# Optimization experiments

Hardware: AMD Instinct MI355X
Metric: run time of the kernel (lower is better)

The kernel has to match this reference:

```python
import jax, jax.numpy as jnp
import numpy as np

B, S, HID = 2, 2048, 1024
H, D = 16, 64
NUM_BUCKETS, MAX_DIST = 32, 128
NEG_INF = -1e9


def _rel_buckets(rel_pos, num_buckets, max_distance):
    # decoder (unidirectional): only non-positive relative positions valid
    rp = -jnp.minimum(rel_pos, 0)  # [q,k] >= 0
    max_exact = num_buckets // 2
    is_small = rp < max_exact
    safe = jnp.maximum(rp, 1).astype(jnp.float32)
    large = max_exact + (
        jnp.log(safe / max_exact) / np.log(max_distance / max_exact) * (num_buckets - max_exact)
    ).astype(jnp.int32)
    large = jnp.minimum(large, num_buckets - 1)
    return jnp.where(is_small, rp, large)


def _rotate_half(t):
    t1, t2 = jnp.split(t, 2, axis=-1)
    return jnp.concatenate([-t2, t1], axis=-1)


def setup_inputs() -> dict:
    key = jax.random.key(0)
    ks = jax.random.split(key, 6)
    sc = 0.02
    x = jax.random.normal(ks[0], (B, S, HID), jnp.float32)
    Wq = jax.random.normal(ks[1], (HID, H * D), jnp.float32) * sc
    Wk = jax.random.normal(ks[2], (HID, H * D), jnp.float32) * sc
    Wv = jax.random.normal(ks[3], (HID, H * D), jnp.float32) * sc
    Wo = jax.random.normal(ks[4], (H * D, HID), jnp.float32) * sc
    rel_bias = jax.random.normal(ks[5], (NUM_BUCKETS, H), jnp.float32) * sc
    # rotary tables: emb = cat(freqs, freqs), non-interleave layout
    inv_freq = 1.0 / (10000.0 ** (np.arange(0, D, 2, dtype=np.float32) / D))
    freqs = np.arange(S, dtype=np.float32)[:, None] * inv_freq[None, :]  # [S, D/2]
    emb = np.concatenate([freqs, freqs], axis=-1)  # [S, D]
    cos = jnp.asarray(np.cos(emb), jnp.float32)
    sin = jnp.asarray(np.sin(emb), jnp.float32)
    return {"x": x, "Wq": Wq, "Wk": Wk, "Wv": Wv, "Wo": Wo,
            "rel_bias": rel_bias, "cos": cos, "sin": sin}


def reference(x, Wq, Wk, Wv, Wo, rel_bias, cos, sin):
    # QKV projections (weights stored [in, out])
    q = (x @ Wq).reshape(B, S, H, D)
    k = (x @ Wk).reshape(B, S, H, D)
    v = (x @ Wv).reshape(B, S, H, D)
    # RoPE (non-interleave): q*cos + rotate_half(q)*sin, cos/sin broadcast over B,H
    c = cos[None, :, None, :]
    s = sin[None, :, None, :]
    q = q * c + _rotate_half(q) * s
    k = k * c + _rotate_half(k) * s
    # scores [B,H,S,S]
    scores = jnp.einsum("bqhd,bkhd->bhqk", q, k) / np.sqrt(D).astype(np.float32)
    # learned relative-position bucket bias (T5-style, decoder/unidirectional)
    ctx_pos = jnp.arange(S)[:, None]
    mem_pos = jnp.arange(S)[None, :]
    buckets = _rel_buckets(mem_pos - ctx_pos, NUM_BUCKETS, MAX_DIST)  # [S,S]
    bias = rel_bias[buckets]  # [S,S,H]
    scores = scores + jnp.transpose(bias, (2, 0, 1))[None]
    # causal mask (decoder self-attention)
    causal = mem_pos <= ctx_pos  # [S,S]
    scores = jnp.where(causal[None, None], scores, NEG_INF)
    attn = jax.nn.softmax(scores, axis=-1)
    ctx = jnp.einsum("bhqk,bkhd->bqhd", attn, v).reshape(B, S, H * D)
    return ctx @ Wo
```

## Files before the change

kernel.cpp:

```cpp
#include <hip/hip_runtime.h>
#include <hip/hip_bf16.h>
#include <math.h>

#define B_   2
#define S_   2048
#define HID_ 1024
#define H_   16
#define D_   64

typedef __attribute__((ext_vector_type(8))) short bf16x8;
typedef __attribute__((ext_vector_type(4))) short bf16x4;
typedef __attribute__((ext_vector_type(4))) float f32x4;
typedef __attribute__((ext_vector_type(4))) unsigned uint4v;
typedef unsigned short u16;

#define LOG2E 1.44269504088896f

static __device__ __forceinline__ u16 f2bf(float f) {
    unsigned u = __builtin_bit_cast(unsigned, f);
    u += 0x7fffu + ((u >> 16) & 1u);
    return (u16)(u >> 16);
}
static __device__ __forceinline__ unsigned cvtpk(float lo, float hi) {
    unsigned r;
    asm("v_cvt_pk_bf16_f32 %0, %1, %2" : "=v"(r) : "v"(lo), "v"(hi));
    return r;
}
static __device__ __forceinline__ int swzK(int row, int colbytes) {
    return row * 128 + (colbytes ^ ((row & 7) << 4));
}
static __device__ __forceinline__ int swzV(int row, int colbytes) {
    return row * 128 + (colbytes ^ ((row & 7) << 4) ^ (((row >> 3) & 1) << 3));
}
static __device__ __forceinline__ void gll16(const void* g, void* l) {
    __builtin_amdgcn_global_load_lds(
        (const __attribute__((address_space(1))) unsigned int*)g,
        (__attribute__((address_space(3))) unsigned int*)l, 16, 0, 0);
}

__global__ __launch_bounds__(256) void convert_x(const float* __restrict__ in,
                                                 u16* __restrict__ out) {
    int i = blockIdx.x * 256 + threadIdx.x;
    float4 f = ((const float4*)in)[i];
    ushort4 u;
    u.x = f2bf(f.x); u.y = f2bf(f.y); u.z = f2bf(f.z); u.w = f2bf(f.w);
    ((ushort4*)out)[i] = u;
}

__global__ __launch_bounds__(256) void transpose_w4(const float* __restrict__ W0,
                                                    const float* __restrict__ W1,
                                                    const float* __restrict__ W2,
                                                    const float* __restrict__ W3,
                                                    u16* __restrict__ o0,
                                                    u16* __restrict__ o1,
                                                    u16* __restrict__ o2,
                                                    u16* __restrict__ o3) {
    __shared__ float tS[32][33];
    const int z = blockIdx.z;
    const float* in = z == 0 ? W0 : z == 1 ? W1 : z == 2 ? W2 : W3;
    u16* out       = z == 0 ? o0 : z == 1 ? o1 : z == 2 ? o2 : o3;
    const int x = threadIdx.x, y = threadIdx.y;
    const int bx = blockIdx.x * 32, by = blockIdx.y * 32;
    #pragma unroll
    for (int j = 0; j < 4; j++)
        tS[y + j * 8][x] = in[(long)(by + y + j * 8) * HID_ + bx + x];
    __syncthreads();
    #pragma unroll
    for (int j = 0; j < 4; j++)
        out[(long)(bx + y + j * 8) * HID_ + by + x] = f2bf(tS[x][y + j * 8]);
}

__global__ __launch_bounds__(256, 3) void gemm_qkv(const u16* __restrict__ A,
                                                   const u16* __restrict__ Bt,
                                                   u16* __restrict__ outb,
                                                   const float* __restrict__ cosb,
                                                   const float* __restrict__ sinb,
                                                   int K) {
    __shared__ u16 As[128 * 32];
    __shared__ u16 Bs[128 * 32];
    const int t = threadIdx.x;
    const int lane = t & 63;
    const int w = t >> 6;
    const int qlane = lane & 15, grp = lane >> 4;
    const int m0 = blockIdx.y * 128, n0 = blockIdx.x * 128;
    const int wr = w >> 1, wc = w & 1;

    f32x4 acc[4][4];
    #pragma unroll
    for (int i = 0; i < 4; i++)
        #pragma unroll
        for (int j = 0; j < 4; j++) acc[i][j] = (f32x4){0.f, 0.f, 0.f, 0.f};

    const int srow = (lane >> 2);
    const int scol = (lane & 3) * 8;
    const int nkt = K >> 5;
    for (int kt = 0; kt < nkt; kt++) {
        const int k0 = kt << 5;
        #pragma unroll
        for (int c = 0; c < 2; c++) {
            const int chunk = w * 2 + c;
            const int row = chunk * 16 + srow;
            gll16(A  + (long)(m0 + row) * K + k0 + scol, As + chunk * 512);
            gll16(Bt + (long)(n0 + row) * K + k0 + scol, Bs + chunk * 512);
        }
        __syncthreads();
        bf16x8 af[4], bfr[4];
        #pragma unroll
        for (int i = 0; i < 4; i++) {
            af[i]  = *(const bf16x8*)(As + (wr * 64 + i * 16 + qlane) * 32 + grp * 8);
            bfr[i] = *(const bf16x8*)(Bs + (wc * 64 + i * 16 + qlane) * 32 + grp * 8);
        }
        #pragma unroll
        for (int mf = 0; mf < 4; mf++)
            #pragma unroll
            for (int nf = 0; nf < 4; nf++)
                acc[mf][nf] = __builtin_amdgcn_mfma_f32_16x16x32_bf16(af[mf], bfr[nf], acc[mf][nf], 0, 0, 0);
        __syncthreads();
    }

    const int gnb = n0 + wc * 64;
    #pragma unroll
    for (int mf = 0; mf < 4; mf++) {
        #pragma unroll
        for (int r = 0; r < 4; r++) {
            const int m = m0 + wr * 64 + mf * 16 + grp * 4 + r;
            float a0 = acc[mf][0][r], a1 = acc[mf][1][r];
            float a2 = acc[mf][2][r], a3 = acc[mf][3][r];
            if (gnb < 2048) {
                const int s = m & (S_ - 1);
                const float* cr = cosb + s * 64;
                const float* sr = sinb + s * 64;
                float c0 = cr[qlane], c1 = cr[qlane + 16], c2 = cr[qlane + 32], c3 = cr[qlane + 48];
                float z0 = sr[qlane], z1 = sr[qlane + 16], z2 = sr[qlane + 32], z3 = sr[qlane + 48];
                float n0v = a0 * c0 - a2 * z0;
                float n1v = a1 * c1 - a3 * z1;
                float n2v = a2 * c2 + a0 * z2;
                float n3v = a3 * c3 + a1 * z3;
                if (gnb < 1024) {
                    const float QS = 0.125f * LOG2E;
                    n0v *= QS; n1v *= QS; n2v *= QS; n3v *= QS;
                }
                a0 = n0v; a1 = n1v; a2 = n2v; a3 = n3v;
            }
            const float av[4] = {a0, a1, a2, a3};
            #pragma unroll
            for (int nf = 0; nf < 4; nf++) {
                const int gn = gnb + nf * 16 + qlane;
                outb[((long)(gn >> 10)) * ((long)4096 * 1024) + (long)m * 1024 + (gn & 1023)]
                    = f2bf(av[nf]);
            }
        }
    }
}

__global__ __launch_bounds__(256, 3) void gemm_n64(const u16* __restrict__ A,
                                                   const u16* __restrict__ Bt,
                                                   float* __restrict__ outf,
                                                   int K) {
    __shared__ u16 As[128 * 32];
    __shared__ u16 Bs[64 * 32];
    const int t = threadIdx.x;
    const int lane = t & 63;
    const int w = t >> 6;
    const int qlane = lane & 15, grp = lane >> 4;
    const int m0 = blockIdx.y * 128, n0 = blockIdx.x * 64;

    f32x4 acc[2][4];
    #pragma unroll
    for (int i = 0; i < 2; i++)
        #pragma unroll
        for (int j = 0; j < 4; j++) acc[i][j] = (f32x4){0.f, 0.f, 0.f, 0.f};

    const int srow = (lane >> 2);
    const int scol = (lane & 3) * 8;
    const int nkt = K >> 5;
    for (int kt = 0; kt < nkt; kt++) {
        const int k0 = kt << 5;
        #pragma unroll
        for (int c = 0; c < 2; c++) {
            const int chunk = w * 2 + c;
            const int row = chunk * 16 + srow;
            gll16(A + (long)(m0 + row) * K + k0 + scol, As + chunk * 512);
        }
        gll16(Bt + (long)(n0 + w * 16 + srow) * K + k0 + scol, Bs + w * 512);
        __syncthreads();
        bf16x8 af[2], bfr[4];
        #pragma unroll
        for (int i = 0; i < 2; i++)
            af[i] = *(const bf16x8*)(As + (w * 32 + i * 16 + qlane) * 32 + grp * 8);
        #pragma unroll
        for (int i = 0; i < 4; i++)
            bfr[i] = *(const bf16x8*)(Bs + (i * 16 + qlane) * 32 + grp * 8);
        #pragma unroll
        for (int mf = 0; mf < 2; mf++)
            #pragma unroll
            for (int nf = 0; nf < 4; nf++)
                acc[mf][nf] = __builtin_amdgcn_mfma_f32_16x16x32_bf16(af[mf], bfr[nf], acc[mf][nf], 0, 0, 0);
        __syncthreads();
    }

    #pragma unroll
    for (int mf = 0; mf < 2; mf++)
        #pragma unroll
        for (int r = 0; r < 4; r++) {
            const int m = m0 + w * 32 + mf * 16 + grp * 4 + r;
            #pragma unroll
            for (int nf = 0; nf < 4; nf++)
                outf[(long)m * 1024 + n0 + nf * 16 + qlane] = acc[mf][nf][r];
        }
}

__global__ __launch_bounds__(512, 4) void attn_mfma(const u16* __restrict__ q,
                                                    const u16* __restrict__ k,
                                                    const u16* __restrict__ v,
                                                    const float* __restrict__ rel_bias,
                                                    u16* __restrict__ ctx) {
    __shared__ __align__(16) unsigned char kS[2][8192];
    __shared__ __align__(16) unsigned char vS[2][8192];
    __shared__ float bb[2][192];

    const int t    = threadIdx.x;
    const int lane = t & 63;
    const int w    = t >> 6;
    const int n    = blockIdx.x;
    const int xcd  = n & 7;
    const int hbhi = (n >> 7) & 3;
    int qtb        = (n >> 3) & 15;
    if (hbhi & 2) qtb = 15 - qtb;
    const int hb   = xcd + (hbhi << 3);
    const int h    = hb & 15, b = hb >> 4;
    const int q0   = qtb * 128;
    const int wq   = w * 16;
    const int qlane = lane & 15;
    const int grp   = lane >> 4;

    const long bhbase = ((long)b * S_ * H_ + h) * D_;
    const float bfar  = rel_bias[31 * H_ + h] * LOG2E;

    const int kr  = t >> 3,        kc  = (t & 7) * 8;
    const int vrb = (t >> 5) * 4,  vcp = (t & 31) * 2;

    bf16x8 qf0, qf1;
    {
        const u16* qrow = q + bhbase + (long)(q0 + wq + qlane) * (H_ * D_);
        qf0 = *(const bf16x8*)(qrow + grp * 8);
        qf1 = *(const bf16x8*)(qrow + 32 + grp * 8);
    }

    f32x4 oacc[4];
    #pragma unroll
    for (int db = 0; db < 4; db++) oacc[db] = (f32x4){0.f, 0.f, 0.f, 0.f};
    float m_run = -1.0e30f, l_run = 0.f;

    bf16x8 kreg;
    unsigned vreg[4];
    float breg = 0.f;

    auto prefetch = [&](int k0, bool needb) {
        kreg = *(const bf16x8*)(k + bhbase + (long)(k0 + kr) * (H_ * D_) + kc);
        const u16* vp = v + bhbase + (long)(k0 + vrb) * (H_ * D_) + vcp;
        #pragma unroll
        for (int i = 0; i < 4; i++)
            vreg[i] = *(const unsigned*)(vp + (long)i * (H_ * D_));
        if (needb && t < 192) {
            int rp = (q0 - 63) + t - k0;
            float bv = 0.f;
            if (rp >= 0) {
                int bucket;
                if (rp < 16) bucket = rp;
                else {
                    int lg = (int)(logf((float)rp * 0.0625f) * 7.69437361f);
                    bucket = 16 + lg;
                    if (bucket > 31) bucket = 31;
                }
                bv = rel_bias[bucket * H_ + h] * LOG2E;
            }
            breg = bv;
        }
    };
    auto writetile = [&](int buf, bool needb) {
        *(bf16x8*)(kS[buf] + swzK(kr, kc * 2)) = kreg;
        ushort2 a0 = __builtin_bit_cast(ushort2, vreg[0]);
        ushort2 a1 = __builtin_bit_cast(ushort2, vreg[1]);
        ushort2 a2 = __builtin_bit_cast(ushort2, vreg[2]);
        ushort2 a3 = __builtin_bit_cast(ushort2, vreg[3]);
        ushort4 d0; d0.x = a0.x; d0.y = a1.x; d0.z = a2.x; d0.w = a3.x;
        ushort4 d1; d1.x = a0.y; d1.y = a1.y; d1.z = a2.y; d1.w = a3.y;
        *(ushort4*)(vS[buf] + swzV(vcp,     vrb * 2)) = d0;
        *(ushort4*)(vS[buf] + swzV(vcp + 1, vrb * 2)) = d1;
        if (needb && t < 192) bb[buf][t] = breg;
    };

    const int NT = 2 * qtb + 2;
    const bool needb0 = (q0 < 176);
    prefetch(0, needb0);
    writetile(0, needb0);
    __syncthreads();

    int cur = 0;
    for (int kt = 0; kt < NT; kt++) {
        const int k0 = kt * 64;
        const bool has_next = (kt + 1) < NT;
        const bool needb_n  = (q0 - (k0 + 64)) < 176;
        if (has_next) prefetch(k0 + 64, needb_n);

        const bool skip = k0 > q0 + wq + 15;
        if (!skip) {
            const bool use_bias = (q0 + wq - k0) < 176;
            const bool is_diag  = (k0 + 63) > (q0 + wq);

            __builtin_amdgcn_s_setprio(1);
            f32x4 sacc[4];
            #pragma unroll
            for (int kb = 0; kb < 4; kb++) {
                sacc[kb] = (f32x4){0.f, 0.f, 0.f, 0.f};
                bf16x8 kf0 = *(const bf16x8*)(kS[cur] + swzK(kb * 16 + qlane, grp * 16));
                bf16x8 kf1 = *(const bf16x8*)(kS[cur] + swzK(kb * 16 + qlane, 64 + grp * 16));
                sacc[kb] = __builtin_amdgcn_mfma_f32_16x16x32_bf16(kf0, qf0, sacc[kb], 0, 0, 0);
                sacc[kb] = __builtin_amdgcn_mfma_f32_16x16x32_bf16(kf1, qf1, sacc[kb], 0, 0, 0);
            }
            __builtin_amdgcn_s_setprio(0);

            float pv_[4][4];
            float tmax = -1.0e30f;
            #pragma unroll
            for (int kb = 0; kb < 4; kb++) {
                #pragma unroll
                for (int r = 0; r < 4; r++) {
                    float s = sacc[kb][r];
                    if (use_bias) {
                        const int k_l = kb * 16 + grp * 4 + r;
                        s += bb[cur][wq + qlane - k_l + 63];
                        if (is_diag)
                            s = ((k0 + k_l) <= (q0 + wq + qlane)) ? s : -1.0e9f;
                    }
                    pv_[kb][r] = s;
                }
                tmax = fmaxf(tmax,
                       fmaxf(fmaxf(pv_[kb][0], pv_[kb][1]), fmaxf(pv_[kb][2], pv_[kb][3])));
            }
            tmax = fmaxf(tmax, __shfl_xor(tmax, 16));
            tmax = fmaxf(tmax, __shfl_xor(tmax, 32));

            const float bofs = use_bias ? 0.f : bfar;
            const float teff = tmax + bofs;
            float msub;
            if (__all(teff <= m_run + 11.5f)) {
                msub = m_run - bofs;
            } else {
                float mnew  = fmaxf(m_run, teff);
                float scale = __builtin_amdgcn_exp2f(m_run - mnew);
                l_run *= scale;
                float scl[4];
                #pragma unroll
                for (int r = 0; r < 4; r++) scl[r] = __shfl(scale, grp * 4 + r, 64);
                #pragma unroll
                for (int db = 0; db < 4; db++)
                    #pragma unroll
                    for (int r = 0; r < 4; r++) oacc[db][r] *= scl[r];
                m_run = mnew;
                msub = mnew - bofs;
            }

            float tsum = 0.f;
            #pragma unroll
            for (int kb = 0; kb < 4; kb++)
                #pragma unroll
                for (int r = 0; r < 4; r++) {
                    float p = __builtin_amdgcn_exp2f(pv_[kb][r] - msub);
                    pv_[kb][r] = p;
                    tsum += p;
                }
            tsum += __shfl_xor(tsum, 16);
            tsum += __shfl_xor(tsum, 32);
            l_run += tsum;

            bf16x8 pf[2];
            #pragma unroll
            for (int ks = 0; ks < 2; ks++) {
                unsigned u0 = cvtpk(pv_[2 * ks][0], pv_[2 * ks][1]);
                unsigned u1 = cvtpk(pv_[2 * ks][2], pv_[2 * ks][3]);
                unsigned u2 = cvtpk(pv_[2 * ks + 1][0], pv_[2 * ks + 1][1]);
                unsigned u3 = cvtpk(pv_[2 * ks + 1][2], pv_[2 * ks + 1][3]);
                pf[ks] = __builtin_bit_cast(bf16x8, (uint4v){u0, u1, u2, u3});
            }

            __builtin_amdgcn_s_setprio(1);
            #pragma unroll
            for (int db = 0; db < 4; db++) {
                #pragma unroll
                for (int ks = 0; ks < 2; ks++) {
                    bf16x4 lo = *(const bf16x4*)(vS[cur] + swzV(db * 16 + qlane, ks * 64 + grp * 8));
                    bf16x4 hi = *(const bf16x4*)(vS[cur] + swzV(db * 16 + qlane, ks * 64 + 32 + grp * 8));
                    bf16x8 vf = __builtin_shufflevector(lo, hi, 0, 1, 2, 3, 4, 5, 6, 7);
                    oacc[db] = __builtin_amdgcn_mfma_f32_16x16x32_bf16(pf[ks], vf, oacc[db], 0, 0, 0);
                }
            }
            __builtin_amdgcn_s_setprio(0);
        }

        if (has_next) writetile(cur ^ 1, needb_n);
        __syncthreads();
        cur ^= 1;
    }

    float inv = 1.0f / l_run;
    float invr[4];
    #pragma unroll
    for (int r = 0; r < 4; r++) invr[r] = __shfl(inv, grp * 4 + r, 64);
    #pragma unroll
    for (int r = 0; r < 4; r++) {
        long qg = q0 + wq + grp * 4 + r;
        u16* dst = ctx + (long)(b * S_ + qg) * HID_ + h * D_ + qlane;
        #pragma unroll
        for (int db = 0; db < 4; db++)
            dst[db * 16] = f2bf(oacc[db][r] * invr[r]);
    }
}

extern "C" void kernel_launch(void* const* d_in, const int* in_sizes, int n_in,
                              void* d_out, int out_size, void* d_ws, size_t ws_size,
                              hipStream_t stream) {
    const float* x    = (const float*)d_in[0];
    const float* Wq   = (const float*)d_in[1];
    const float* Wk   = (const float*)d_in[2];
    const float* Wv   = (const float*)d_in[3];
    const float* Wo   = (const float*)d_in[4];
    const float* rb   = (const float*)d_in[5];
    const float* cosb = (const float*)d_in[6];
    const float* sinb = (const float*)d_in[7];
    float* out = (float*)d_out;

    char* wsb = (char*)d_ws;
    u16* xb    = (u16*)(wsb);
    u16* wqkvT = (u16*)(wsb + (8L  << 20));
    u16* woT   = (u16*)(wsb + (14L << 20));
    u16* qb    = (u16*)(wsb + (16L << 20));
    u16* kb    = (u16*)(wsb + (24L << 20));
    u16* vb    = (u16*)(wsb + (32L << 20));
    u16* ctxb  = (u16*)(wsb + (40L << 20));

    hipLaunchKernelGGL(convert_x, dim3((B_ * S_ * HID_ / 4) / 256), dim3(256), 0, stream, x, xb);
    hipLaunchKernelGGL(transpose_w4, dim3(32, 32, 4), dim3(32, 8), 0, stream,
                       Wq, Wk, Wv, Wo,
                       wqkvT, wqkvT + (1L << 20), wqkvT + (2L << 20), woT);

    hipLaunchKernelGGL(gemm_qkv, dim3(24, 32), dim3(256), 0, stream,
                       xb, wqkvT, qb, cosb, sinb, HID_);
    hipLaunchKernelGGL(attn_mfma, dim3(512), dim3(512), 0, stream,
                       qb, kb, vb, rb, ctxb);
    hipLaunchKernelGGL(gemm_n64, dim3(16, 32), dim3(256), 0, stream,
                       ctxb, woT, out, HID_);
}
```

Baseline: 121.4 us.

## Process key tiles in pairs and transpose MFMA outputs for vectorized stores

The attention kernel now loads two 64-key tiles per iteration into doubled shared buffers, so it synchronizes and prefetches half as often, with a wider bias window. The MFMA operands are swapped in the GEMMs and in the PV product, so each lane's accumulator holds consecutive columns of one row. This removes the cross-lane shuffles for the softmax rescale and normalization and allows 4-wide vector global stores. Shared memory per block and register use go up, which may lower occupancy.

```diff
diff --git a/kernel.cpp b/kernel.cpp
--- a/kernel.cpp
+++ b/kernel.cpp
@@ -114,41 +114,42 @@
         for (int mf = 0; mf < 4; mf++)
             #pragma unroll
             for (int nf = 0; nf < 4; nf++)
-                acc[mf][nf] = __builtin_amdgcn_mfma_f32_16x16x32_bf16(af[mf], bfr[nf], acc[mf][nf], 0, 0, 0);
+                acc[mf][nf] = __builtin_amdgcn_mfma_f32_16x16x32_bf16(bfr[nf], af[mf], acc[mf][nf], 0, 0, 0);
         __syncthreads();
     }
 
     const int gnb = n0 + wc * 64;
+    const bool isqk = gnb < 2048;
+    const bool isq  = gnb < 1024;
+    const float QS = 0.125f * LOG2E;
     #pragma unroll
     for (int mf = 0; mf < 4; mf++) {
-        #pragma unroll
-        for (int r = 0; r < 4; r++) {
-            const int m = m0 + wr * 64 + mf * 16 + grp * 4 + r;
-            float a0 = acc[mf][0][r], a1 = acc[mf][1][r];
-            float a2 = acc[mf][2][r], a3 = acc[mf][3][r];
-            if (gnb < 2048) {
-                const int s = m & (S_ - 1);
-                const float* cr = cosb + s * 64;
-                const float* sr = sinb + s * 64;
-                float c0 = cr[qlane], c1 = cr[qlane + 16], c2 = cr[qlane + 32], c3 = cr[qlane + 48];
-                float z0 = sr[qlane], z1 = sr[qlane + 16], z2 = sr[qlane + 32], z3 = sr[qlane + 48];
-                float n0v = a0 * c0 - a2 * z0;
-                float n1v = a1 * c1 - a3 * z1;
-                float n2v = a2 * c2 + a0 * z2;
-                float n3v = a3 * c3 + a1 * z3;
-                if (gnb < 1024) {
-                    const float QS = 0.125f * LOG2E;
-                    n0v *= QS; n1v *= QS; n2v *= QS; n3v *= QS;
+        const int m = m0 + wr * 64 + mf * 16 + qlane;
+        if (isqk) {
+            const int s = m & (S_ - 1);
+            const float* cr = cosb + s * 64;
+            const float* sr = sinb + s * 64;
+            #pragma unroll
+            for (int nf2 = 0; nf2 < 2; nf2++) {
+                #pragma unroll
+                for (int r = 0; r < 4; r++) {
+                    const int d = nf2 * 16 + grp * 4 + r;
+                    float lo = acc[mf][nf2][r], hi = acc[mf][nf2 + 2][r];
+                    float nlo = lo * cr[d]      - hi * sr[d];
+                    float nhi = hi * cr[d + 32] + lo * sr[d + 32];
+                    if (isq) { nlo *= QS; nhi *= QS; }
+                    acc[mf][nf2][r]     = nlo;
+                    acc[mf][nf2 + 2][r] = nhi;
                 }
-                a0 = n0v; a1 = n1v; a2 = n2v; a3 = n3v;
-            }
-            const float av[4] = {a0, a1, a2, a3};
-            #pragma unroll
-            for (int nf = 0; nf < 4; nf++) {
-                const int gn = gnb + nf * 16 + qlane;
-                outb[((long)(gn >> 10)) * ((long)4096 * 1024) + (long)m * 1024 + (gn & 1023)]
-                    = f2bf(av[nf]);
-            }
+            }
+        }
+        #pragma unroll
+        for (int nf = 0; nf < 4; nf++) {
+            const int gn = gnb + nf * 16 + grp * 4;
+            ushort4 o4;
+            o4.x = f2bf(acc[mf][nf][0]); o4.y = f2bf(acc[mf][nf][1]);
+            o4.z = f2bf(acc[mf][nf][2]); o4.w = f2bf(acc[mf][nf][3]);
+            *(ushort4*)&outb[((long)(gn >> 10)) * ((long)4096 * 1024) + (long)m * 1024 + (gn & 1023)] = o4;
         }
     }
 }
@@ -195,19 +196,21 @@
         for (int mf = 0; mf < 2; mf++)
             #pragma unroll
             for (int nf = 0; nf < 4; nf++)
-                acc[mf][nf] = __builtin_amdgcn_mfma_f32_16x16x32_bf16(af[mf], bfr[nf], acc[mf][nf], 0, 0, 0);
+                acc[mf][nf] = __builtin_amdgcn_mfma_f32_16x16x32_bf16(bfr[nf], af[mf], acc[mf][nf], 0, 0, 0);
         __syncthreads();
     }
 
     #pragma unroll
-    for (int mf = 0; mf < 2; mf++)
-        #pragma unroll
-        for (int r = 0; r < 4; r++) {
-            const int m = m0 + w * 32 + mf * 16 + grp * 4 + r;
-            #pragma unroll
-            for (int nf = 0; nf < 4; nf++)
-                outf[(long)m * 1024 + n0 + nf * 16 + qlane] = acc[mf][nf][r];
-        }
+    for (int mf = 0; mf < 2; mf++) {
+        const int m = m0 + w * 32 + mf * 16 + qlane;
+        #pragma unroll
+        for (int nf = 0; nf < 4; nf++) {
+            float4 o4;
+            o4.x = acc[mf][nf][0]; o4.y = acc[mf][nf][1];
+            o4.z = acc[mf][nf][2]; o4.w = acc[mf][nf][3];
+            *(float4*)&outf[(long)m * 1024 + n0 + nf * 16 + grp * 4] = o4;
+        }
+    }
 }
 
 __global__ __launch_bounds__(512, 4) void attn_mfma(const u16* __restrict__ q,
@@ -215,9 +218,9 @@
                                                     const u16* __restrict__ v,
                                                     const float* __restrict__ rel_bias,
                                                     u16* __restrict__ ctx) {
-    __shared__ __align__(16) unsigned char kS[2][8192];
-    __shared__ __align__(16) unsigned char vS[2][8192];
-    __shared__ float bb[2][192];
+    __shared__ __align__(16) unsigned char kS[2][2][8192];
+    __shared__ __align__(16) unsigned char vS[2][2][8192];
+    __shared__ float bb[2][256];
 
     const int t    = threadIdx.x;
     const int lane = t & 63;
@@ -231,6 +234,7 @@
     const int h    = hb & 15, b = hb >> 4;
     const int q0   = qtb * 128;
     const int wq   = w * 16;
+    const int qwq  = q0 + wq;
     const int qlane = lane & 15;
     const int grp   = lane >> 4;
 
@@ -242,7 +246,7 @@
 
     bf16x8 qf0, qf1;
     {
-        const u16* qrow = q + bhbase + (long)(q0 + wq + qlane) * (H_ * D_);
+        const u16* qrow = q + bhbase + (long)(qwq + qlane) * (H_ * D_);
         qf0 = *(const bf16x8*)(qrow + grp * 8);
         qf1 = *(const bf16x8*)(qrow + 32 + grp * 8);
     }
@@ -252,18 +256,22 @@
     for (int db = 0; db < 4; db++) oacc[db] = (f32x4){0.f, 0.f, 0.f, 0.f};
     float m_run = -1.0e30f, l_run = 0.f;
 
-    bf16x8 kreg;
-    unsigned vreg[4];
+    bf16x8 kregA, kregB;
+    unsigned vreg[8];
     float breg = 0.f;
 
-    auto prefetch = [&](int k0, bool needb) {
-        kreg = *(const bf16x8*)(k + bhbase + (long)(k0 + kr) * (H_ * D_) + kc);
-        const u16* vp = v + bhbase + (long)(k0 + vrb) * (H_ * D_) + vcp;
-        #pragma unroll
-        for (int i = 0; i < 4; i++)
-            vreg[i] = *(const unsigned*)(vp + (long)i * (H_ * D_));
-        if (needb && t < 192) {
-            int rp = (q0 - 63) + t - k0;
+    auto prefetch = [&](int k0p, bool needb) {
+        const u16* kp = k + bhbase + (long)(k0p + kr) * (H_ * D_) + kc;
+        kregA = *(const bf16x8*)kp;
+        kregB = *(const bf16x8*)(kp + (long)64 * (H_ * D_));
+        const u16* vp = v + bhbase + (long)(k0p + vrb) * (H_ * D_) + vcp;
+        #pragma unroll
+        for (int i = 0; i < 4; i++) {
+            vreg[i]     = *(const unsigned*)(vp + (long)i * (H_ * D_));
+            vreg[i + 4] = *(const unsigned*)(vp + (long)(i + 64) * (H_ * D_));
+        }
+        if (needb && t < 256) {
+            int rp = q0 - k0p - 127 + t;
             float bv = 0.f;
             if (rp >= 0) {
                 int bucket;
@@ -279,47 +287,65 @@
         }
     };
     auto writetile = [&](int buf, bool needb) {
-        *(bf16x8*)(kS[buf] + swzK(kr, kc * 2)) = kreg;
-        ushort2 a0 = __builtin_bit_cast(ushort2, vreg[0]);
-        ushort2 a1 = __builtin_bit_cast(ushort2, vreg[1]);
-        ushort2 a2 = __builtin_bit_cast(ushort2, vreg[2]);
-        ushort2 a3 = __builtin_bit_cast(ushort2, vreg[3]);
-        ushort4 d0; d0.x = a0.x; d0.y = a1.x; d0.z = a2.x; d0.w = a3.x;
-        ushort4 d1; d1.x = a0.y; d1.y = a1.y; d1.z = a2.y; d1.w = a3.y;
-        *(ushort4*)(vS[buf] + swzV(vcp,     vrb * 2)) = d0;
-        *(ushort4*)(vS[buf] + swzV(vcp + 1, vrb * 2)) = d1;
-        if (needb && t < 192) bb[buf][t] = breg;
+        *(bf16x8*)(kS[buf][0] + swzK(kr, kc * 2)) = kregA;
+        *(bf16x8*)(kS[buf][1] + swzK(kr, kc * 2)) = kregB;
+        #pragma unroll
+        for (int s = 0; s < 2; s++) {
+            ushort2 a0 = __builtin_bit_cast(ushort2, vreg[s * 4 + 0]);
+            ushort2 a1 = __builtin_bit_cast(ushort2, vreg[s * 4 + 1]);
+            ushort2 a2 = __builtin_bit_cast(ushort2, vreg[s * 4 + 2]);
+            ushort2 a3 = __builtin_bit_cast(ushort2, vreg[s * 4 + 3]);
+            ushort4 d0; d0.x = a0.x; d0.y = a1.x; d0.z = a2.x; d0.w = a3.x;
+            ushort4 d1; d1.x = a0.y; d1.y = a1.y; d1.z = a2.y; d1.w = a3.y;
+            *(ushort4*)(vS[buf][s] + swzV(vcp,     vrb * 2)) = d0;
+            *(ushort4*)(vS[buf][s] + swzV(vcp + 1, vrb * 2)) = d1;
+        }
+        if (needb && t < 256) bb[buf][t] = breg;
     };
 
-    const int NT = 2 * qtb + 2;
-    const bool needb0 = (q0 < 176);
-    prefetch(0, needb0);
-    writetile(0, needb0);
+    const int NPAIR = qtb + 1;
+    prefetch(0, (q0 - 0) < 256);
+    writetile(0, (q0 - 0) < 256);
     __syncthreads();
 
     int cur = 0;
-    for (int kt = 0; kt < NT; kt++) {
-        const int k0 = kt * 64;
-        const bool has_next = (kt + 1) < NT;
-        const bool needb_n  = (q0 - (k0 + 64)) < 176;
-        if (has_next) prefetch(k0 + 64, needb_n);
-
-        const bool skip = k0 > q0 + wq + 15;
-        if (!skip) {
-            const bool use_bias = (q0 + wq - k0) < 176;
-            const bool is_diag  = (k0 + 63) > (q0 + wq);
-
-            __builtin_amdgcn_s_setprio(1);
-            f32x4 sacc[4];
+    for (int pr = 0; pr < NPAIR; pr++) {
+        const int k0p = pr * 128;
+        const bool has_next = (pr + 1) < NPAIR;
+        const bool needb_n  = (q0 - (k0p + 128)) < 256;
+        if (has_next) prefetch(k0p + 128, needb_n);
+
+        const bool skipB = (k0p + 64) > qwq + 15;
+
+        __builtin_amdgcn_s_setprio(1);
+        f32x4 saccA[4], saccB[4];
+        #pragma unroll
+        for (int kb = 0; kb < 4; kb++) {
+            saccA[kb] = (f32x4){0.f, 0.f, 0.f, 0.f};
+            bf16x8 kf0 = *(const bf16x8*)(kS[cur][0] + swzK(kb * 16 + qlane, grp * 16));
+            bf16x8 kf1 = *(const bf16x8*)(kS[cur][0] + swzK(kb * 16 + qlane, 64 + grp * 16));
+            saccA[kb] = __builtin_amdgcn_mfma_f32_16x16x32_bf16(kf0, qf0, saccA[kb], 0, 0, 0);
+            saccA[kb] = __builtin_amdgcn_mfma_f32_16x16x32_bf16(kf1, qf1, saccA[kb], 0, 0, 0);
+        }
+        if (!skipB) {
             #pragma unroll
             for (int kb = 0; kb < 4; kb++) {
-                sacc[kb] = (f32x4){0.f, 0.f, 0.f, 0.f};
-                bf16x8 kf0 = *(const bf16x8*)(kS[cur] + swzK(kb * 16 + qlane, grp * 16));
-                bf16x8 kf1 = *(const bf16x8*)(kS[cur] + swzK(kb * 16 + qlane, 64 + grp * 16));
-                sacc[kb] = __builtin_amdgcn_mfma_f32_16x16x32_bf16(kf0, qf0, sacc[kb], 0, 0, 0);
-                sacc[kb] = __builtin_amdgcn_mfma_f32_16x16x32_bf16(kf1, qf1, sacc[kb], 0, 0, 0);
-            }
-            __builtin_amdgcn_s_setprio(0);
+                saccB[kb] = (f32x4){0.f, 0.f, 0.f, 0.f};
+                bf16x8 kf0 = *(const bf16x8*)(kS[cur][1] + swzK(kb * 16 + qlane, grp * 16));
+                bf16x8 kf1 = *(const bf16x8*)(kS[cur][1] + swzK(kb * 16 + qlane, 64 + grp * 16));
+                saccB[kb] = __builtin_amdgcn_mfma_f32_16x16x32_bf16(kf0, qf0, saccB[kb], 0, 0, 0);
+                saccB[kb] = __builtin_amdgcn_mfma_f32_16x16x32_bf16(kf1, qf1, saccB[kb], 0, 0, 0);
+            }
+        }
+        __builtin_amdgcn_s_setprio(0);
+
+        #pragma unroll
+        for (int sub = 0; sub < 2; sub++) {
+            if (sub == 1 && skipB) break;
+            const int k0s = k0p + sub * 64;
+            const bool use_bias = (qwq - k0s) < 176;
+            const bool is_diag  = (k0s + 63) > qwq;
+            f32x4* sacc = (sub == 0) ? saccA : saccB;
 
             float pv_[4][4];
             float tmax = -1.0e30f;
@@ -330,9 +356,9 @@
                     float s = sacc[kb][r];
                     if (use_bias) {
                         const int k_l = kb * 16 + grp * 4 + r;
-                        s += bb[cur][wq + qlane - k_l + 63];
+                        s += bb[cur][wq + qlane - sub * 64 - k_l + 127];
                         if (is_diag)
-                            s = ((k0 + k_l) <= (q0 + wq + qlane)) ? s : -1.0e9f;
+                            s = ((k0s + k_l) <= (qwq + qlane)) ? s : -1.0e9f;
                     }
                     pv_[kb][r] = s;
                 }
@@ -351,13 +377,10 @@
                 float mnew  = fmaxf(m_run, teff);
                 float scale = __builtin_amdgcn_exp2f(m_run - mnew);
                 l_run *= scale;
-                float scl[4];
-                #pragma unroll
-                for (int r = 0; r < 4; r++) scl[r] = __shfl(scale, grp * 4 + r, 64);
                 #pragma unroll
                 for (int db = 0; db < 4; db++)
                     #pragma unroll
-                    for (int r = 0; r < 4; r++) oacc[db][r] *= scl[r];
+                    for (int r = 0; r < 4; r++) oacc[db][r] *= scale;
                 m_run = mnew;
                 msub = mnew - bofs;
             }
@@ -390,10 +413,10 @@
             for (int db = 0; db < 4; db++) {
                 #pragma unroll
                 for (int ks = 0; ks < 2; ks++) {
-                    bf16x4 lo = *(const bf16x4*)(vS[cur] + swzV(db * 16 + qlane, ks * 64 + grp * 8));
-                    bf16x4 hi = *(const bf16x4*)(vS[cur] + swzV(db * 16 + qlane, ks * 64 + 32 + grp * 8));
+                    bf16x4 lo = *(const bf16x4*)(vS[cur][sub] + swzV(db * 16 + qlane, ks * 64 + grp * 8));
+                    bf16x4 hi = *(const bf16x4*)(vS[cur][sub] + swzV(db * 16 + qlane, ks * 64 + 32 + grp * 8));
                     bf16x8 vf = __builtin_shufflevector(lo, hi, 0, 1, 2, 3, 4, 5, 6, 7);
-                    oacc[db] = __builtin_amdgcn_mfma_f32_16x16x32_bf16(pf[ks], vf, oacc[db], 0, 0, 0);
+                    oacc[db] = __builtin_amdgcn_mfma_f32_16x16x32_bf16(vf, pf[ks], oacc[db], 0, 0, 0);
                 }
             }
             __builtin_amdgcn_s_setprio(0);
@@ -404,17 +427,16 @@
         cur ^= 1;
     }
 
-    float inv = 1.0f / l_run;
-    float invr[4];
-    #pragma unroll
-    for (int r = 0; r < 4; r++) invr[r] = __shfl(inv, grp * 4 + r, 64);
-    #pragma unroll
-    for (int r = 0; r < 4; r++) {
-        long qg = q0 + wq + grp * 4 + r;
-        u16* dst = ctx + (long)(b * S_ + qg) * HID_ + h * D_ + qlane;
-        #pragma unroll
-        for (int db = 0; db < 4; db++)
-            dst[db * 16] = f2bf(oacc[db][r] * invr[r]);
+    const float inv = 1.0f / l_run;
+    u16* dst = ctx + (long)(b * S_ + qwq + qlane) * HID_ + h * D_;
+    #pragma unroll
+    for (int db = 0; db < 4; db++) {
+        ushort4 o4;
+        o4.x = f2bf(oacc[db][0] * inv);
+        o4.y = f2bf(oacc[db][1] * inv);
+        o4.z = f2bf(oacc[db][2] * inv);
+        o4.w = f2bf(oacc[db][3] * inv);
+        *(ushort4*)(dst + db * 16 + grp * 4) = o4;
     }
 }
 
```

After: 141.4 us. 1.17x slower.
